# Kernel optimization log

Hardware: AMD Instinct MI355X
Metric: run time of the kernel (lower is better)

Reference implementation:

```python
import jax, jax.numpy as jnp
import numpy as np

G = 16       # groups
GRID = 25    # hardcoded self.grid
EPS = 1e-5   # BatchNorm eps


def _gconv(x, w, pad):
    # x: (B, Cin, H, W), w: (Cout, Cin//G, kh, kw); grouped conv, stride 1
    return jax.lax.conv_general_dilated(
        x, w, window_strides=(1, 1), padding=[(pad, pad), (pad, pad)],
        feature_group_count=G)


def _bn_relu(h, g, b, m, v):
    # h: (G, B, C, H, W); per-group-instance BN params: (G, C). Inference BN.
    scale = (g / jnp.sqrt(v + EPS))[:, None, :, None, None]
    return jax.nn.relu((h - m[:, None, :, None, None]) * scale + b[:, None, :, None, None])


def setup_inputs() -> dict:
    key = jax.random.key(0)
    ks = jax.random.split(key, 11)
    B, C, H, W = 2, 256, 24, 24
    AC = GRID * C  # 6400 affinity channels
    return {
        "x":  jax.random.normal(ks[0], (B, C, H, W), jnp.float32),
        "W1": jax.random.normal(ks[1], (G, C, C // G, 3, 3), jnp.float32) * 0.05,
        "g1": jax.random.uniform(ks[2], (G, C), jnp.float32, 0.5, 1.5),
        "b1": jax.random.normal(ks[3], (G, C), jnp.float32) * 0.1,
        "m1": jax.random.normal(ks[4], (G, C), jnp.float32) * 0.1,
        "v1": jax.random.uniform(ks[5], (G, C), jnp.float32, 0.5, 1.5),
        "W2": jax.random.normal(ks[6], (G, AC, C // G, 1, 1), jnp.float32) * 0.05,
        "g2": jax.random.uniform(ks[7], (G, AC), jnp.float32, 0.5, 1.5),
        "b2": jax.random.normal(ks[8], (G, AC), jnp.float32) * 0.1,
        "m2": jax.random.normal(ks[9], (G, AC), jnp.float32) * 0.1,
        "v2": jax.random.uniform(ks[10], (G, AC), jnp.float32, 0.5, 1.5),
    }


def reference(x, W1, g1, b1, m1, v1, W2, g2, b2, m2, v2):
    B, C, H, W = x.shape
    Cg = C // G
    # 16 independent grouped 3x3 convs over the same input, batched via vmap
    h1 = jax.vmap(lambda w: _gconv(x, w, 1))(W1)          # (G, B, C, H, W)
    h1 = _bn_relu(h1, g1, b1, m1, v1)
    # grouped 1x1 conv with padding=1 (faithful to source -> spatial grows to H+2, W+2)
    a = jax.vmap(lambda h, w: _gconv(h, w, 1))(h1, W2)    # (G, B, 25C, H+2, W+2)
    a = _bn_relu(a, g2, b2, m2, v2)
    pooled = a.mean(axis=(-2, -1))                        # adaptive avg pool -> (G, B, 25C)
    xv = pooled.reshape(G, B, G, GRID * Cg)               # (G, B, G, 25*Cg)
    aff = jnp.einsum('ibkm,iblm->ibkl', xv, xv)           # (G, B, G, G) = theta @ phi
    idx = jnp.arange(G)
    aff_i = aff[idx, :, idx, :] / G                       # aff[:, i], /N  -> (G, B, G)
    ex = h1.reshape(G, B, G, Cg * H * W)
    # torch.matmul((B,G), (B,G,M)) broadcasts 2-D lhs -> (B, B, M); kept faithfully
    z = jnp.einsum('ipk,iqkm->ipqm', aff_i, ex)           # (G, B, B, Cg*H*W)
    z = z.reshape(G, B, B, Cg, H, W).transpose(1, 0, 2, 3, 4, 5)
    return z.reshape(B, G * B * Cg, H, W)                 # (B, B*C, H, W)
```

## Files before the change

kernel.cpp:

```cpp
#include <hip/hip_runtime.h>
#include <hip/hip_bf16.h>


typedef __attribute__((ext_vector_type(8))) short short8;
typedef __attribute__((ext_vector_type(4))) short short4v;
typedef __attribute__((ext_vector_type(4))) float f32x4;

static __device__ __forceinline__ short f2bf(float x) {
    unsigned u = __float_as_uint(x);
    unsigned r = (u + 0x7fffu + ((u >> 16) & 1u)) >> 16;
    return (short)r;
}

#define WA_OFF  33696
#define WLB_OFF 23040
#define B2_OFF  35840
#define PS_OFF  37440
#define ZP_OFF  43840
#define SMEM_BYTES 43856

__global__ __launch_bounds__(256) void k12_fused(
    const float* __restrict__ xin,
    const float* __restrict__ W1,
    const float* __restrict__ g1, const float* __restrict__ b1,
    const float* __restrict__ m1, const float* __restrict__ v1,
    const float* __restrict__ W2,
    const float* __restrict__ g2, const float* __restrict__ b2,
    const float* __restrict__ m2, const float* __restrict__ v2,
    float* __restrict__ h1f,
    float* __restrict__ pooled)
{
    __shared__ __align__(16) char smem[SMEM_BYTES];
    short* xs    = (short*)smem;
    short* wAp   = (short*)(smem + WA_OFF);
    short* hsb   = (short*)smem;
    short* wlb   = (short*)(smem + WLB_OFF);
    float* bias2 = (float*)(smem + B2_OFF);
    float* psum  = (float*)(smem + PS_OFF);
    __shared__ float scale1[16], bias1[16];

    int bid = blockIdx.x;
    int i = bid >> 5, b = (bid >> 4) & 1, g = bid & 15;
    int t = threadIdx.x;

    int* xz = (int*)xs;
    for (int idx = t; idx < 27*26*12; idx += 256) xz[idx] = 0;
    if (t < 4) ((int*)(smem + ZP_OFF))[t] = 0;
    if (t < 16) {
        int c = i*256 + g*16 + t;
        float sc = g1[c] * rsqrtf(v1[c] + 1e-5f);
        scale1[t] = sc;
        bias1[t]  = b1[c] - m1[c] * sc;
    }
    __syncthreads();

    const float* xb = &xin[(b*256 + g*16)*576];
    for (int idx = t; idx < 9216; idx += 256) {
        int ci = idx / 576; int s = idx - ci*576;
        int y = s / 24; int x = s - y*24;
        xs[((y+1)*26 + (x+1))*24 + ci] = f2bf(xb[idx]);
    }
    const float* wb = &W1[(i*256 + g*16)*144];
    for (int idx = t; idx < 2560; idx += 256) {
        int kk = idx >> 9, rem = idx & 511, co = rem >> 5, k = rem & 31;
        int tap = 2*kk + (k >> 4), ci = k & 15;
        float val = (tap < 9) ? wb[co*144 + ci*9 + tap] * scale1[co] : 0.f;
        wAp[(kk*16 + co)*40 + k] = f2bf(val);
    }
    __syncthreads();

    int l = t & 63, w = t >> 6;
    int quad = l >> 4, rc = l & 15;

    f32x4 dreg[9];
    {
        int ci0 = (quad & 1) * 8;
        short8 afr[5];
#pragma unroll
        for (int kk = 0; kk < 5; kk++)
            afr[kk] = *(const short8*)&wAp[(kk*16 + rc)*40 + quad*8];
        f32x4 cb1 = *(const f32x4*)&bias1[quad*4];

        const int offE[5] = {0, 48, 648, 1248, 1296};
        const int offO[5] = {24, 624, 672, 1272, 1872};
        int off[5];
#pragma unroll
        for (int kk = 0; kk < 5; kk++) off[kk] = (quad >= 2) ? offO[kk] : offE[kk];

#pragma unroll
        for (int tt = 0; tt < 9; tt++) {
            int s = (w*9 + tt)*16 + rc;
            int y = s / 24; int x = s - y*24;
            int base = (y*26 + x)*24 + ci0;
            f32x4 acc = cb1;
#pragma unroll
            for (int kk = 0; kk < 5; kk++) {
                short8 bf = *(const short8*)&xs[base + off[kk]];
                acc = __builtin_amdgcn_mfma_f32_16x16x32_bf16(afr[kk], bf, acc, 0, 0, 0);
            }
#pragma unroll
            for (int r = 0; r < 4; r++) acc[r] = fmaxf(acc[r], 0.f);
            dreg[tt] = acc;
        }
    }
    __syncthreads();

    {
        float* hout = &h1f[((i*2 + b)*256 + g*16)*576];
#pragma unroll
        for (int tt = 0; tt < 9; tt++) {
            int s = (w*9 + tt)*16 + rc;
            f32x4 acc = dreg[tt];
            unsigned p0 = (unsigned)(unsigned short)f2bf(acc[0]) |
                          ((unsigned)(unsigned short)f2bf(acc[1]) << 16);
            unsigned p1 = (unsigned)(unsigned short)f2bf(acc[2]) |
                          ((unsigned)(unsigned short)f2bf(acc[3]) << 16);
            uint2 pk = {p0, p1};
            *(uint2*)&hsb[s*20 + quad*4] = pk;
#pragma unroll
            for (int r = 0; r < 4; r++)
                hout[(quad*4 + r)*576 + s] = acc[r];
        }
    }

    for (int m = t; m < 400; m += 256) {
        int o = i*6400 + g*400 + m;
        float s2 = g2[o] * rsqrtf(v2[o] + 1e-5f);
        bias2[m] = b2[o] - m2[o] * s2;
        const float4* wr = (const float4*)&W2[o*16];
#pragma unroll
        for (int q = 0; q < 4; q++) {
            float4 wv = wr[q];
            wlb[m*16 + q*4 + 0] = f2bf(wv.x * s2);
            wlb[m*16 + q*4 + 1] = f2bf(wv.y * s2);
            wlb[m*16 + q*4 + 2] = f2bf(wv.z * s2);
            wlb[m*16 + q*4 + 3] = f2bf(wv.w * s2);
        }
    }
    __syncthreads();

    {
        int q8 = (quad & 1) * 8;
        short8 af2[9];
#pragma unroll
        for (int u = 0; u < 9; u++) {
            int boff = (l < 32) ? ((((w*9 + u)*16 + rc)*20 + q8)*2) : ZP_OFF;
            af2[u] = *(const short8*)(smem + boff);
        }
        for (int mt = 0; mt < 25; mt++) {
            int m0 = mt*16;
            int woff = (l < 32) ? (WLB_OFF + ((m0 + rc)*16 + q8)*2) : ZP_OFF;
            short8 wf = *(const short8*)(smem + woff);
            float be = bias2[m0 + rc];
            f32x4 cb = {be, be, be, be};

            f32x4 accv = {0.f, 0.f, 0.f, 0.f};
#pragma unroll
            for (int u = 0; u < 9; u++) {
                f32x4 d = __builtin_amdgcn_mfma_f32_16x16x32_bf16(af2[u], wf, cb, 0, 0, 0);
#pragma unroll
                for (int r = 0; r < 4; r++)
                    accv[r] += fmaxf(d[r], 0.f);
            }
            float a = (accv[0] + accv[1]) + (accv[2] + accv[3]);
            a += __shfl_xor(a, 16);
            a += __shfl_xor(a, 32);
            if (l < 16)
                psum[w*400 + m0 + l] = a;
        }
    }
    __syncthreads();

    const float inv = 1.f / 676.f;
    for (int m = t; m < 400; m += 256) {
        float s = psum[0*400+m] + psum[1*400+m] + psum[2*400+m] + psum[3*400+m];
        float be = bias2[m];
        pooled[(i*2+b)*6400 + g*400 + m] = (s + 100.f * fmaxf(be, 0.f)) * inv;
    }
}

__global__ __launch_bounds__(256) void k3_aff(const float* __restrict__ pooled,
                                              float* __restrict__ aff)
{
    __shared__ float th[400];
    __shared__ float parts[256];
    int bid = blockIdx.x;
    int i = bid >> 1;
    int t = threadIdx.x;
    const float* pb = &pooled[bid*6400];
    for (int idx = t; idx < 400; idx += 256) th[idx] = pb[i*400 + idx];
    __syncthreads();
    int l = t >> 4, p = t & 15;
    float sum = 0.f;
    const float* pl = &pb[l*400];
    for (int m = p*25; m < p*25 + 25; m++) sum = fmaf(th[m], pl[m], sum);
    parts[t] = sum;
    __syncthreads();
    if (t < 16) {
        float s = 0.f;
        for (int pp = 0; pp < 16; pp++) s += parts[t*16 + pp];
        aff[bid*16 + t] = s * (1.f/16.f);
    }
}

__global__ __launch_bounds__(256) void k4_out(const float* __restrict__ h1f,
                                              const float* __restrict__ aff,
                                              float* __restrict__ out)
{
    __shared__ float a0[16], a1[16];
    int bid = blockIdx.x;
    int i = bid >> 5, q = (bid >> 4) & 1, cg = bid & 15;
    int t = threadIdx.x;
    if (t < 16) a0[t] = aff[(i*2+0)*16 + t];
    else if (t < 32) a1[t-16] = aff[(i*2+1)*16 + (t-16)];
    __syncthreads();
    const float* hb = &h1f[((i*2+q)*256 + cg)*576];
    int ch = i*32 + q*16 + cg;
    for (int s = t; s < 576; s += 256) {
        float acc0 = 0.f, acc1 = 0.f;
#pragma unroll
        for (int k = 0; k < 16; k++) {
            float v = hb[k*9216 + s];
            acc0 = fmaf(a0[k], v, acc0);
            acc1 = fmaf(a1[k], v, acc1);
        }
        out[ch*576 + s]         = acc0;
        out[(512 + ch)*576 + s] = acc1;
    }
}

extern "C" void kernel_launch(void* const* d_in, const int* in_sizes, int n_in,
                              void* d_out, int out_size, void* d_ws, size_t ws_size,
                              hipStream_t stream)
{
    const float* x  = (const float*)d_in[0];
    const float* W1 = (const float*)d_in[1];
    const float* g1 = (const float*)d_in[2];
    const float* b1 = (const float*)d_in[3];
    const float* m1 = (const float*)d_in[4];
    const float* v1 = (const float*)d_in[5];
    const float* W2 = (const float*)d_in[6];
    const float* g2 = (const float*)d_in[7];
    const float* b2 = (const float*)d_in[8];
    const float* m2 = (const float*)d_in[9];
    const float* v2 = (const float*)d_in[10];

    float* h1f    = (float*)d_ws;
    float* pooled = h1f + 16*2*256*576;
    float* aff    = pooled + 16*2*6400;

    float* out = (float*)d_out;

    hipLaunchKernelGGL(k12_fused, dim3(512), dim3(256), 0, stream,
                       x, W1, g1, b1, m1, v1, W2, g2, b2, m2, v2, h1f, pooled);
    hipLaunchKernelGGL(k3_aff,    dim3(32),  dim3(256), 0, stream,
                       pooled, aff);
    hipLaunchKernelGGL(k4_out,    dim3(512), dim3(256), 0, stream,
                       h1f, aff, out);
}
```

Measured before the change: 117.5 us.

## Split fused conv kernel over affinity-channel halves and fold affinity into output kernel

The first kernel now launches twice as many blocks. Each pair recomputes the 3x3 grouped conv but handles only half of the 400 affinity output channels in the 1x1 conv and pooling stage, and only one of the pair writes h1. The separate affinity kernel is removed, and each output block recomputes its two affinity rows from pooled before the weighted sum. This aims to raise occupancy across CUs and drop one launch. The cost is duplicated conv work in the first kernel and redundant affinity dot products in every output block.

```diff
diff --git a/kernel.cpp b/kernel.cpp
--- a/kernel.cpp
+++ b/kernel.cpp
@@ -3,7 +3,6 @@
 
 
 typedef __attribute__((ext_vector_type(8))) short short8;
-typedef __attribute__((ext_vector_type(4))) short short4v;
 typedef __attribute__((ext_vector_type(4))) float f32x4;
 
 static __device__ __forceinline__ short f2bf(float x) {
@@ -39,8 +38,10 @@
     float* psum  = (float*)(smem + PS_OFF);
     __shared__ float scale1[16], bias1[16];
 
-    int bid = blockIdx.x;
-    int i = bid >> 5, b = (bid >> 4) & 1, g = bid & 15;
+    int bid  = blockIdx.x;
+    int hsel = bid & 1;
+    int core = bid >> 1;
+    int i = core >> 5, b = (core >> 4) & 1, g = core & 15;
     int t = threadIdx.x;
 
     int* xz = (int*)xs;
@@ -117,13 +118,17 @@
                           ((unsigned)(unsigned short)f2bf(acc[3]) << 16);
             uint2 pk = {p0, p1};
             *(uint2*)&hsb[s*20 + quad*4] = pk;
-#pragma unroll
-            for (int r = 0; r < 4; r++)
-                hout[(quad*4 + r)*576 + s] = acc[r];
-        }
-    }
-
-    for (int m = t; m < 400; m += 256) {
+            if (hsel == 0) {
+#pragma unroll
+                for (int r = 0; r < 4; r++)
+                    hout[(quad*4 + r)*576 + s] = acc[r];
+            }
+        }
+    }
+
+    int m_lo = hsel ? 208 : 0;
+    int m_hi = hsel ? 400 : 208;
+    for (int m = m_lo + t; m < m_hi; m += 256) {
         int o = i*6400 + g*400 + m;
         float s2 = g2[o] * rsqrtf(v2[o] + 1e-5f);
         bias2[m] = b2[o] - m2[o] * s2;
@@ -147,7 +152,9 @@
             int boff = (l < 32) ? ((((w*9 + u)*16 + rc)*20 + q8)*2) : ZP_OFF;
             af2[u] = *(const short8*)(smem + boff);
         }
-        for (int mt = 0; mt < 25; mt++) {
+        int mt_lo = hsel ? 13 : 0;
+        int mt_hi = hsel ? 25 : 13;
+        for (int mt = mt_lo; mt < mt_hi; mt++) {
             int m0 = mt*16;
             int woff = (l < 32) ? (WLB_OFF + ((m0 + rc)*16 + q8)*2) : ZP_OFF;
             short8 wf = *(const short8*)(smem + woff);
@@ -172,57 +179,52 @@
     __syncthreads();
 
     const float inv = 1.f / 676.f;
-    for (int m = t; m < 400; m += 256) {
+    for (int m = m_lo + t; m < m_hi; m += 256) {
         float s = psum[0*400+m] + psum[1*400+m] + psum[2*400+m] + psum[3*400+m];
         float be = bias2[m];
         pooled[(i*2+b)*6400 + g*400 + m] = (s + 100.f * fmaxf(be, 0.f)) * inv;
     }
 }
 
-__global__ __launch_bounds__(256) void k3_aff(const float* __restrict__ pooled,
-                                              float* __restrict__ aff)
+__global__ __launch_bounds__(256) void k34_out(const float* __restrict__ pooled,
+                                               const float* __restrict__ h1f,
+                                               float* __restrict__ out)
 {
-    __shared__ float th[400];
     __shared__ float parts[256];
-    int bid = blockIdx.x;
-    int i = bid >> 1;
-    int t = threadIdx.x;
-    const float* pb = &pooled[bid*6400];
-    for (int idx = t; idx < 400; idx += 256) th[idx] = pb[i*400 + idx];
-    __syncthreads();
-    int l = t >> 4, p = t & 15;
-    float sum = 0.f;
-    const float* pl = &pb[l*400];
-    for (int m = p*25; m < p*25 + 25; m++) sum = fmaf(th[m], pl[m], sum);
-    parts[t] = sum;
-    __syncthreads();
-    if (t < 16) {
-        float s = 0.f;
-        for (int pp = 0; pp < 16; pp++) s += parts[t*16 + pp];
-        aff[bid*16 + t] = s * (1.f/16.f);
-    }
-}
-
-__global__ __launch_bounds__(256) void k4_out(const float* __restrict__ h1f,
-                                              const float* __restrict__ aff,
-                                              float* __restrict__ out)
-{
-    __shared__ float a0[16], a1[16];
+    __shared__ float av[2][16];
     int bid = blockIdx.x;
     int i = bid >> 5, q = (bid >> 4) & 1, cg = bid & 15;
     int t = threadIdx.x;
-    if (t < 16) a0[t] = aff[(i*2+0)*16 + t];
-    else if (t < 32) a1[t-16] = aff[(i*2+1)*16 + (t-16)];
-    __syncthreads();
-    const float* hb = &h1f[((i*2+q)*256 + cg)*576];
+
+    {
+        int pl = t >> 3;
+        int u  = t & 7;
+        int p = pl >> 4, lidx = pl & 15;
+        const float* pb = &pooled[(i*2 + p)*6400];
+        const float* pt = &pb[i*400];
+        const float* pl2 = &pb[lidx*400];
+        float s = 0.f;
+        for (int m = u*50; m < u*50 + 50; m++) s = fmaf(pt[m], pl2[m], s);
+        parts[t] = s;
+    }
+    __syncthreads();
+    if (t < 32) {
+        float s = 0.f;
+#pragma unroll
+        for (int u = 0; u < 8; u++) s += parts[t*8 + u];
+        av[t >> 4][t & 15] = s * (1.f/16.f);
+    }
+    __syncthreads();
+
+    const float* hb = &h1f[((i*2 + q)*256 + cg)*576];
     int ch = i*32 + q*16 + cg;
     for (int s = t; s < 576; s += 256) {
         float acc0 = 0.f, acc1 = 0.f;
 #pragma unroll
         for (int k = 0; k < 16; k++) {
             float v = hb[k*9216 + s];
-            acc0 = fmaf(a0[k], v, acc0);
-            acc1 = fmaf(a1[k], v, acc1);
+            acc0 = fmaf(av[0][k], v, acc0);
+            acc1 = fmaf(av[1][k], v, acc1);
         }
         out[ch*576 + s]         = acc0;
         out[(512 + ch)*576 + s] = acc1;
@@ -247,14 +249,11 @@
 
     float* h1f    = (float*)d_ws;
     float* pooled = h1f + 16*2*256*576;
-    float* aff    = pooled + 16*2*6400;
 
     float* out = (float*)d_out;
 
-    hipLaunchKernelGGL(k12_fused, dim3(512), dim3(256), 0, stream,
+    hipLaunchKernelGGL(k12_fused, dim3(1024), dim3(256), 0, stream,
                        x, W1, g1, b1, m1, v1, W2, g2, b2, m2, v2, h1f, pooled);
-    hipLaunchKernelGGL(k3_aff,    dim3(32),  dim3(256), 0, stream,
-                       pooled, aff);
-    hipLaunchKernelGGL(k4_out,    dim3(512), dim3(256), 0, stream,
-                       h1f, aff, out);
-}
+    hipLaunchKernelGGL(k34_out,   dim3(512),  dim3(256), 0, stream,
+                       pooled, h1f, out);
+}
```

After: 125.8 us. 1.07x slower.
